# Kernel optimization log

Measured on AMD Instinct MI355X. Metric: run time of the kernel, lower is better.

The kernel has to match this reference:

```python
import jax, jax.numpy as jnp
import numpy as np

N = 8192
IN_F = 256
OUT_F = 256
ATTN_DIM = 2
NEG_INF = -1e18


def setup_inputs() -> dict:
    key = jax.random.key(0)
    k1, k2, k3, k4, k5 = jax.random.split(key, 5)
    node_feats = jax.random.normal(k1, (N, IN_F), dtype=jnp.float32)
    Ahat = (jax.random.uniform(k2, (N, N)) < 0.01).astype(jnp.float32)
    # ensure no isolated rows (self loops) so softmax rows are well-defined
    Ahat = Ahat.at[jnp.arange(N), jnp.arange(N)].set(1.0)
    bound_w = 1.0 / np.sqrt(IN_F)
    bound_wa = 1.0 / np.sqrt(OUT_F)
    bound_a = 1.0 / np.sqrt(2 * ATTN_DIM)
    w = jax.random.uniform(k3, (IN_F, OUT_F), minval=-bound_w, maxval=bound_w, dtype=jnp.float32)
    w_a = jax.random.uniform(k4, (OUT_F, ATTN_DIM), minval=-bound_wa, maxval=bound_wa, dtype=jnp.float32)
    a = jax.random.uniform(k5, (2 * ATTN_DIM, 1), minval=-bound_a, maxval=bound_a, dtype=jnp.float32)
    return {"node_feats": node_feats, "Ahat": Ahat, "w": w, "w_a": w_a, "a": a}


def reference(node_feats, Ahat, w, w_a, a):
    # h_prime: [N, out_features]
    h_prime = node_feats @ w
    # h_reduced: [N, attn_dim]
    h_reduced = h_prime @ w_a
    # e[i, j] = cat(h_red[i], h_red[j]) @ a  ==  h_red[i]@a[:d] + h_red[j]@a[d:]
    # (identical math to the repeat+cat+matmul in the original, without the
    #  O(N^2 * 2d) materialization)
    f_src = (h_reduced @ a[:ATTN_DIM]).squeeze(-1)  # [N]
    f_dst = (h_reduced @ a[ATTN_DIM:]).squeeze(-1)  # [N]
    e = f_src[:, None] + f_dst[None, :]             # [N, N]
    masked_e = jnp.where(Ahat > 0, e, NEG_INF)
    attn_scores = jax.nn.softmax(masked_e, axis=-1)  # [N, N]
    out = attn_scores @ h_prime                      # [N, out_features]
    return jax.nn.relu(out)
```

## Files before the change

kernel.cpp:

```cpp
#include <hip/hip_runtime.h>
#include <hip/hip_bf16.h>
#include <math.h>

#define NN 8192
#define IN_F 256
#define OUT_F 256

#define KC 32
#define AS_STRIDE 68
#define BS_STRIDE 132

__global__ __launch_bounds__(256) void gemm_hprime(
    const float* __restrict__ X,
    const float* __restrict__ W,
    float* __restrict__ H)
{
    __shared__ float As[KC * AS_STRIDE];
    __shared__ float Bs[KC * BS_STRIDE];

    const int tid  = threadIdx.x;
    const int row0 = blockIdx.x * 64;
    const int col0 = blockIdx.y * 128;
    const int tx   = tid & 15;
    const int ty   = tid >> 4;

    float acc[4][8];
#pragma unroll
    for (int i = 0; i < 4; ++i)
#pragma unroll
        for (int j = 0; j < 8; ++j) acc[i][j] = 0.0f;

    for (int k0 = 0; k0 < IN_F; k0 += KC) {
        {
            const int k4    = tid & 7;
            const int rbase = tid >> 3;
#pragma unroll
            for (int rp = 0; rp < 2; ++rp) {
                const int r = rbase + rp * 32;
                const float4 v = *(const float4*)(X + (size_t)(row0 + r) * IN_F + k0 + k4 * 4);
                As[(k4 * 4 + 0) * AS_STRIDE + r] = v.x;
                As[(k4 * 4 + 1) * AS_STRIDE + r] = v.y;
                As[(k4 * 4 + 2) * AS_STRIDE + r] = v.z;
                As[(k4 * 4 + 3) * AS_STRIDE + r] = v.w;
            }
        }
        {
            const int c4 = tid & 31;
            const int kb = tid >> 5;
#pragma unroll
            for (int kp = 0; kp < 4; ++kp) {
                const int k = kb + kp * 8;
                *(float4*)(&Bs[k * BS_STRIDE + c4 * 4]) =
                    *(const float4*)(W + (size_t)(k0 + k) * OUT_F + col0 + c4 * 4);
            }
        }
        __syncthreads();

#pragma unroll
        for (int k = 0; k < KC; ++k) {
            const float4 av = *(const float4*)(&As[k * AS_STRIDE + ty * 4]);
            const float4 b0 = *(const float4*)(&Bs[k * BS_STRIDE + tx * 8]);
            const float4 b1 = *(const float4*)(&Bs[k * BS_STRIDE + tx * 8 + 4]);
            const float a_[4] = {av.x, av.y, av.z, av.w};
            const float b_[8] = {b0.x, b0.y, b0.z, b0.w, b1.x, b1.y, b1.z, b1.w};
#pragma unroll
            for (int i = 0; i < 4; ++i)
#pragma unroll
                for (int j = 0; j < 8; ++j)
                    acc[i][j] = fmaf(a_[i], b_[j], acc[i][j]);
        }
        __syncthreads();
    }

#pragma unroll
    for (int i = 0; i < 4; ++i) {
        float* dst = H + (size_t)(row0 + ty * 4 + i) * OUT_F + col0 + tx * 8;
        float4 o0 = {acc[i][0], acc[i][1], acc[i][2], acc[i][3]};
        float4 o1 = {acc[i][4], acc[i][5], acc[i][6], acc[i][7]};
        *(float4*)(dst)     = o0;
        *(float4*)(dst + 4) = o1;
    }
}

__global__ __launch_bounds__(256) void fdst_exp(
    const float* __restrict__ hp,
    const float* __restrict__ w_a,
    const float* __restrict__ a,
    float* __restrict__ fexp)
{
    const int row  = blockIdx.x * 4 + (threadIdx.x >> 6);
    const int lane = threadIdx.x & 63;

    const float a2 = a[2];
    const float a3 = a[3];

    const float4 h   = *(const float4*)(hp + (size_t)row * OUT_F + lane * 4);
    const float4 wa0 = *(const float4*)(w_a + lane * 8);
    const float4 wa1 = *(const float4*)(w_a + lane * 8 + 4);

    float s = h.x * fmaf(wa0.x, a2, wa0.y * a3)
            + h.y * fmaf(wa0.z, a2, wa0.w * a3)
            + h.z * fmaf(wa1.x, a2, wa1.y * a3)
            + h.w * fmaf(wa1.z, a2, wa1.w * a3);

#pragma unroll
    for (int off = 32; off > 0; off >>= 1) s += __shfl_xor(s, off, 64);

    if (lane == 0) fexp[row] = expf(s);
}

#define CAP 1024

__global__ __launch_bounds__(256) void attn_aggregate(
    const float* __restrict__ Ahat,
    const float* __restrict__ hp,
    const float* __restrict__ fexp,
    float* __restrict__ out)
{
    const int row = blockIdx.x;
    const int tid = threadIdx.x;

    __shared__ int   s_cnt;
    __shared__ int   s_idx[CAP];
    __shared__ float s_p[CAP];

    if (tid == 0) s_cnt = 0;
    __syncthreads();

    const float4* arow = (const float4*)(Ahat + (size_t)row * NN);
#pragma unroll
    for (int it = 0; it < 8; ++it) {
        const int v4 = tid + it * 256;
        const float4 v = arow[v4];
        const int j0 = v4 * 4;
        if (v.x > 0.0f) { int p = atomicAdd(&s_cnt, 1); if (p < CAP) { s_idx[p] = j0 + 0; s_p[p] = fexp[j0 + 0]; } }
        if (v.y > 0.0f) { int p = atomicAdd(&s_cnt, 1); if (p < CAP) { s_idx[p] = j0 + 1; s_p[p] = fexp[j0 + 1]; } }
        if (v.z > 0.0f) { int p = atomicAdd(&s_cnt, 1); if (p < CAP) { s_idx[p] = j0 + 2; s_p[p] = fexp[j0 + 2]; } }
        if (v.w > 0.0f) { int p = atomicAdd(&s_cnt, 1); if (p < CAP) { s_idx[p] = j0 + 3; s_p[p] = fexp[j0 + 3]; } }
    }
    __syncthreads();

    const int cnt = (s_cnt < CAP) ? s_cnt : CAP;

    float acc0 = 0.0f, acc1 = 0.0f, acc2 = 0.0f, acc3 = 0.0f;
    float den = 0.0f;
    int k = 0;
    for (; k + 4 <= cnt; k += 4) {
        const int j0 = s_idx[k + 0], j1 = s_idx[k + 1], j2 = s_idx[k + 2], j3 = s_idx[k + 3];
        const float p0 = s_p[k + 0], p1 = s_p[k + 1], p2 = s_p[k + 2], p3 = s_p[k + 3];
        const float h0 = hp[(size_t)j0 * OUT_F + tid];
        const float h1 = hp[(size_t)j1 * OUT_F + tid];
        const float h2 = hp[(size_t)j2 * OUT_F + tid];
        const float h3 = hp[(size_t)j3 * OUT_F + tid];
        acc0 = fmaf(p0, h0, acc0);
        acc1 = fmaf(p1, h1, acc1);
        acc2 = fmaf(p2, h2, acc2);
        acc3 = fmaf(p3, h3, acc3);
        den += (p0 + p1) + (p2 + p3);
    }
    for (; k < cnt; ++k) {
        const int j = s_idx[k];
        const float p = s_p[k];
        acc0 = fmaf(p, hp[(size_t)j * OUT_F + tid], acc0);
        den += p;
    }

    const float acc = (acc0 + acc1) + (acc2 + acc3);
    out[(size_t)row * OUT_F + tid] = fmaxf(acc / den, 0.0f);
}

extern "C" void kernel_launch(void* const* d_in, const int* in_sizes, int n_in,
                              void* d_out, int out_size, void* d_ws, size_t ws_size,
                              hipStream_t stream) {
    const float* node_feats = (const float*)d_in[0];
    const float* Ahat       = (const float*)d_in[1];
    const float* w          = (const float*)d_in[2];
    const float* w_a        = (const float*)d_in[3];
    const float* a          = (const float*)d_in[4];
    float* out = (float*)d_out;

    float* hp   = (float*)d_ws;
    float* fexp = hp + (size_t)NN * OUT_F;

    gemm_hprime<<<dim3(NN / 64, OUT_F / 128), 256, 0, stream>>>(node_feats, w, hp);

    fdst_exp<<<dim3(NN / 4), 256, 0, stream>>>(hp, w_a, a, fexp);

    attn_aggregate<<<dim3(NN), 256, 0, stream>>>(Ahat, hp, fexp, out);
}
```

Before: 449.5 us.

## Store h_prime in fp16 and aggregate one row per wavefront via ballot

Writes h_prime to the workspace as fp16 instead of fp32, which halves the bytes gathered for every neighbor in the aggregation kernel. The GEMM tile is narrowed to 64 columns to match, and the attention-aggregate kernel is rewritten so that each wavefront owns one row. It scans the adjacency with ballot masks and a prefetched float4 stream, replacing the shared-memory atomic compaction and block-wide syncs. The fp16 storage adds rounding error in h_prime and in the softmax logits.

```diff
diff --git a/kernel.cpp b/kernel.cpp
--- a/kernel.cpp
+++ b/kernel.cpp
@@ -6,51 +6,52 @@
 #define IN_F 256
 #define OUT_F 256
 
+typedef _Float16 half4_t __attribute__((ext_vector_type(4)));
+
 #define KC 32
-#define AS_STRIDE 68
-#define BS_STRIDE 132
+#define LS 68
 
 __global__ __launch_bounds__(256) void gemm_hprime(
     const float* __restrict__ X,
     const float* __restrict__ W,
-    float* __restrict__ H)
+    _Float16* __restrict__ H16)
 {
-    __shared__ float As[KC * AS_STRIDE];
-    __shared__ float Bs[KC * BS_STRIDE];
+    __shared__ float As[KC * LS];
+    __shared__ float Bs[KC * LS];
 
     const int tid  = threadIdx.x;
     const int row0 = blockIdx.x * 64;
-    const int col0 = blockIdx.y * 128;
+    const int col0 = blockIdx.y * 64;
     const int tx   = tid & 15;
     const int ty   = tid >> 4;
 
-    float acc[4][8];
+    float acc[4][4];
 #pragma unroll
     for (int i = 0; i < 4; ++i)
 #pragma unroll
-        for (int j = 0; j < 8; ++j) acc[i][j] = 0.0f;
+        for (int j = 0; j < 4; ++j) acc[i][j] = 0.0f;
 
     for (int k0 = 0; k0 < IN_F; k0 += KC) {
         {
-            const int k4    = tid & 7;
-            const int rbase = tid >> 3;
+            const int k4 = tid & 7;
+            const int r0 = tid >> 3;
 #pragma unroll
             for (int rp = 0; rp < 2; ++rp) {
-                const int r = rbase + rp * 32;
+                const int r = r0 + rp * 32;
                 const float4 v = *(const float4*)(X + (size_t)(row0 + r) * IN_F + k0 + k4 * 4);
-                As[(k4 * 4 + 0) * AS_STRIDE + r] = v.x;
-                As[(k4 * 4 + 1) * AS_STRIDE + r] = v.y;
-                As[(k4 * 4 + 2) * AS_STRIDE + r] = v.z;
-                As[(k4 * 4 + 3) * AS_STRIDE + r] = v.w;
+                As[(k4 * 4 + 0) * LS + r] = v.x;
+                As[(k4 * 4 + 1) * LS + r] = v.y;
+                As[(k4 * 4 + 2) * LS + r] = v.z;
+                As[(k4 * 4 + 3) * LS + r] = v.w;
             }
         }
         {
-            const int c4 = tid & 31;
-            const int kb = tid >> 5;
+            const int c4 = tid & 15;
+            const int kb = tid >> 4;
 #pragma unroll
-            for (int kp = 0; kp < 4; ++kp) {
-                const int k = kb + kp * 8;
-                *(float4*)(&Bs[k * BS_STRIDE + c4 * 4]) =
+            for (int kp = 0; kp < 2; ++kp) {
+                const int k = kb + kp * 16;
+                *(float4*)(&Bs[k * LS + c4 * 4]) =
                     *(const float4*)(W + (size_t)(k0 + k) * OUT_F + col0 + c4 * 4);
             }
         }
@@ -58,15 +59,14 @@
 
 #pragma unroll
         for (int k = 0; k < KC; ++k) {
-            const float4 av = *(const float4*)(&As[k * AS_STRIDE + ty * 4]);
-            const float4 b0 = *(const float4*)(&Bs[k * BS_STRIDE + tx * 8]);
-            const float4 b1 = *(const float4*)(&Bs[k * BS_STRIDE + tx * 8 + 4]);
+            const float4 av = *(const float4*)(&As[k * LS + ty * 4]);
+            const float4 bv = *(const float4*)(&Bs[k * LS + tx * 4]);
             const float a_[4] = {av.x, av.y, av.z, av.w};
-            const float b_[8] = {b0.x, b0.y, b0.z, b0.w, b1.x, b1.y, b1.z, b1.w};
+            const float b_[4] = {bv.x, bv.y, bv.z, bv.w};
 #pragma unroll
             for (int i = 0; i < 4; ++i)
 #pragma unroll
-                for (int j = 0; j < 8; ++j)
+                for (int j = 0; j < 4; ++j)
                     acc[i][j] = fmaf(a_[i], b_[j], acc[i][j]);
         }
         __syncthreads();
@@ -74,16 +74,17 @@
 
 #pragma unroll
     for (int i = 0; i < 4; ++i) {
-        float* dst = H + (size_t)(row0 + ty * 4 + i) * OUT_F + col0 + tx * 8;
-        float4 o0 = {acc[i][0], acc[i][1], acc[i][2], acc[i][3]};
-        float4 o1 = {acc[i][4], acc[i][5], acc[i][6], acc[i][7]};
-        *(float4*)(dst)     = o0;
-        *(float4*)(dst + 4) = o1;
+        half4_t o;
+        o.x = (_Float16)acc[i][0];
+        o.y = (_Float16)acc[i][1];
+        o.z = (_Float16)acc[i][2];
+        o.w = (_Float16)acc[i][3];
+        *(half4_t*)(H16 + (size_t)(row0 + ty * 4 + i) * OUT_F + col0 + tx * 4) = o;
     }
 }
 
 __global__ __launch_bounds__(256) void fdst_exp(
-    const float* __restrict__ hp,
+    const _Float16* __restrict__ hp16,
     const float* __restrict__ w_a,
     const float* __restrict__ a,
     float* __restrict__ fexp)
@@ -94,14 +95,14 @@
     const float a2 = a[2];
     const float a3 = a[3];
 
-    const float4 h   = *(const float4*)(hp + (size_t)row * OUT_F + lane * 4);
+    const half4_t h  = ((const half4_t*)hp16)[(size_t)row * 64 + lane];
     const float4 wa0 = *(const float4*)(w_a + lane * 8);
     const float4 wa1 = *(const float4*)(w_a + lane * 8 + 4);
 
-    float s = h.x * fmaf(wa0.x, a2, wa0.y * a3)
-            + h.y * fmaf(wa0.z, a2, wa0.w * a3)
-            + h.z * fmaf(wa1.x, a2, wa1.y * a3)
-            + h.w * fmaf(wa1.z, a2, wa1.w * a3);
+    float s = (float)h.x * fmaf(wa0.x, a2, wa0.y * a3)
+            + (float)h.y * fmaf(wa0.z, a2, wa0.w * a3)
+            + (float)h.z * fmaf(wa1.x, a2, wa1.y * a3)
+            + (float)h.w * fmaf(wa1.z, a2, wa1.w * a3);
 
 #pragma unroll
     for (int off = 32; off > 0; off >>= 1) s += __shfl_xor(s, off, 64);
@@ -109,64 +110,64 @@
     if (lane == 0) fexp[row] = expf(s);
 }
 
-#define CAP 1024
-
 __global__ __launch_bounds__(256) void attn_aggregate(
     const float* __restrict__ Ahat,
-    const float* __restrict__ hp,
+    const _Float16* __restrict__ hp16,
     const float* __restrict__ fexp,
     float* __restrict__ out)
 {
-    const int row = blockIdx.x;
-    const int tid = threadIdx.x;
+    const int wid  = threadIdx.x >> 6;
+    const int lane = threadIdx.x & 63;
+    const int row  = blockIdx.x * 4 + wid;
 
-    __shared__ int   s_cnt;
-    __shared__ int   s_idx[CAP];
-    __shared__ float s_p[CAP];
+    const float4* arow  = (const float4*)(Ahat + (size_t)row * NN);
+    const half4_t* hp4  = (const half4_t*)hp16;
 
-    if (tid == 0) s_cnt = 0;
-    __syncthreads();
+    float4 acc = {0.0f, 0.0f, 0.0f, 0.0f};
+    float den = 0.0f;
 
-    const float4* arow = (const float4*)(Ahat + (size_t)row * NN);
-#pragma unroll
-    for (int it = 0; it < 8; ++it) {
-        const int v4 = tid + it * 256;
-        const float4 v = arow[v4];
-        const int j0 = v4 * 4;
-        if (v.x > 0.0f) { int p = atomicAdd(&s_cnt, 1); if (p < CAP) { s_idx[p] = j0 + 0; s_p[p] = fexp[j0 + 0]; } }
-        if (v.y > 0.0f) { int p = atomicAdd(&s_cnt, 1); if (p < CAP) { s_idx[p] = j0 + 1; s_p[p] = fexp[j0 + 1]; } }
-        if (v.z > 0.0f) { int p = atomicAdd(&s_cnt, 1); if (p < CAP) { s_idx[p] = j0 + 2; s_p[p] = fexp[j0 + 2]; } }
-        if (v.w > 0.0f) { int p = atomicAdd(&s_cnt, 1); if (p < CAP) { s_idx[p] = j0 + 3; s_p[p] = fexp[j0 + 3]; } }
-    }
-    __syncthreads();
+    float4 v0 = arow[lane];
+    float4 v1 = arow[64 + lane];
 
-    const int cnt = (s_cnt < CAP) ? s_cnt : CAP;
+    for (int c = 0; c < 32; ++c) {
+        const float4 cur = v0;
+        v0 = v1;
+        if (c + 2 < 32) v1 = arow[(c + 2) * 64 + lane];
 
-    float acc0 = 0.0f, acc1 = 0.0f, acc2 = 0.0f, acc3 = 0.0f;
-    float den = 0.0f;
-    int k = 0;
-    for (; k + 4 <= cnt; k += 4) {
-        const int j0 = s_idx[k + 0], j1 = s_idx[k + 1], j2 = s_idx[k + 2], j3 = s_idx[k + 3];
-        const float p0 = s_p[k + 0], p1 = s_p[k + 1], p2 = s_p[k + 2], p3 = s_p[k + 3];
-        const float h0 = hp[(size_t)j0 * OUT_F + tid];
-        const float h1 = hp[(size_t)j1 * OUT_F + tid];
-        const float h2 = hp[(size_t)j2 * OUT_F + tid];
-        const float h3 = hp[(size_t)j3 * OUT_F + tid];
-        acc0 = fmaf(p0, h0, acc0);
-        acc1 = fmaf(p1, h1, acc1);
-        acc2 = fmaf(p2, h2, acc2);
-        acc3 = fmaf(p3, h3, acc3);
-        den += (p0 + p1) + (p2 + p3);
-    }
-    for (; k < cnt; ++k) {
-        const int j = s_idx[k];
-        const float p = s_p[k];
-        acc0 = fmaf(p, hp[(size_t)j * OUT_F + tid], acc0);
-        den += p;
+        const int base = c * 256;
+        unsigned long long m0 = __ballot(cur.x > 0.0f);
+        unsigned long long m1 = __ballot(cur.y > 0.0f);
+        unsigned long long m2 = __ballot(cur.z > 0.0f);
+        unsigned long long m3 = __ballot(cur.w > 0.0f);
+
+#define PROCESS(mask, comp)                                          \
+        while (mask) {                                               \
+            const int b = __builtin_ctzll(mask);                     \
+            mask &= mask - 1;                                        \
+            const int j = base + (b << 2) + (comp);                  \
+            const float p = fexp[j];                                 \
+            const half4_t h = hp4[((size_t)j << 6) + lane];          \
+            acc.x = fmaf(p, (float)h.x, acc.x);                      \
+            acc.y = fmaf(p, (float)h.y, acc.y);                      \
+            acc.z = fmaf(p, (float)h.z, acc.z);                      \
+            acc.w = fmaf(p, (float)h.w, acc.w);                      \
+            den += p;                                                \
+        }
+
+        PROCESS(m0, 0)
+        PROCESS(m1, 1)
+        PROCESS(m2, 2)
+        PROCESS(m3, 3)
+#undef PROCESS
     }
 
-    const float acc = (acc0 + acc1) + (acc2 + acc3);
-    out[(size_t)row * OUT_F + tid] = fmaxf(acc / den, 0.0f);
+    const float inv = 1.0f / den;
+    float4 o;
+    o.x = fmaxf(acc.x * inv, 0.0f);
+    o.y = fmaxf(acc.y * inv, 0.0f);
+    o.z = fmaxf(acc.z * inv, 0.0f);
+    o.w = fmaxf(acc.w * inv, 0.0f);
+    *(float4*)(out + (size_t)row * OUT_F + lane * 4) = o;
 }
 
 extern "C" void kernel_launch(void* const* d_in, const int* in_sizes, int n_in,
@@ -179,12 +180,12 @@
     const float* a          = (const float*)d_in[4];
     float* out = (float*)d_out;
 
-    float* hp   = (float*)d_ws;
-    float* fexp = hp + (size_t)NN * OUT_F;
+    _Float16* hp16 = (_Float16*)d_ws;
+    float* fexp = (float*)(hp16 + (size_t)NN * OUT_F);
 
-    gemm_hprime<<<dim3(NN / 64, OUT_F / 128), 256, 0, stream>>>(node_feats, w, hp);
+    gemm_hprime<<<dim3(NN / 64, OUT_F / 64), 256, 0, stream>>>(node_feats, w, hp16);
 
-    fdst_exp<<<dim3(NN / 4), 256, 0, stream>>>(hp, w_a, a, fexp);
+    fdst_exp<<<dim3(NN / 4), 256, 0, stream>>>(hp16, w_a, a, fexp);
 
-    attn_aggregate<<<dim3(NN), 256, 0, stream>>>(Ahat, hp, fexp, out);
+    attn_aggregate<<<dim3(NN / 4), 256, 0, stream>>>(Ahat, hp16, fexp, out);
 }
```

After: 408.3 us. 9.2% less time.
